# Kernel tuning notes

Hardware: AMD Instinct MI355X
Metric: run time of the kernel (lower is better)

Reference implementation:

```python
import jax, jax.numpy as jnp
import numpy as np

N, F, H, C = 8192, 256, 256, 40
LP = 0.2  # LeakyReLU slope


def setup_inputs() -> dict:
    key = jax.random.key(0)
    ks = jax.random.split(key, 11)
    s = 1.0 / np.sqrt(F)
    return {
        "x": jax.random.normal(ks[0], (N, F), jnp.float32),
        "adj_f": jax.random.uniform(ks[1], (N, N), jnp.float32) / N,
        "adj_a": jax.random.uniform(ks[2], (N, N), jnp.float32) / N,
        "Wp": jax.random.normal(ks[3], (F, F), jnp.float32) * s,
        "bp": jax.random.normal(ks[4], (F,), jnp.float32) * s,
        "Wg": jax.random.normal(ks[5], (F, F), jnp.float32) * s,
        "Wb": jax.random.normal(ks[6], (F, F), jnp.float32) * s,
        "W1": jax.random.normal(ks[7], (F, H), jnp.float32) * s,
        "b1": jax.random.normal(ks[8], (H,), jnp.float32) * s,
        "W2": jax.random.normal(ks[9], (H, C), jnp.float32) * s,
        "b2": jax.random.normal(ks[10], (C,), jnp.float32) * s,
    }


def reference(x, adj_f, adj_a, Wp, bp, Wg, Wb, W1, b1, W2, b2):
    # --- DynamicPrompt.forward ---
    # GraphConvolution: adj_f @ (x @ Wp) + bp, then ReLU
    base_prompt = jax.nn.relu(adj_f @ (x @ Wp) + bp)  # [N, F]
    # adj_a.fill_diagonal_(0)
    idx = jnp.arange(N)
    adj_a0 = adj_a.at[idx, idx].set(0.0)
    neighbor = adj_a0 @ x                             # [N, F]
    gamma = jax.nn.leaky_relu(neighbor @ Wg, LP) + 1.0
    beta = jax.nn.leaky_relu(neighbor @ Wb, LP)
    learned_prompt = gamma * base_prompt + beta
    # F.normalize: L2 along dim=1, eps=1e-12
    nrm = jnp.linalg.norm(learned_prompt, axis=1, keepdims=True)
    learned_prompt = learned_prompt / jnp.maximum(nrm, 1e-12)
    # --- mix prompt into input, run frozen teacher GCN (eval: no dropout) ---
    x_in = 0.5 * (x + learned_prompt)
    h = jax.nn.relu(adj_a @ (x_in @ W1) + b1)         # gc1
    logits = adj_a @ (h @ W2) + b2                    # gc2
    return jax.nn.log_softmax(logits, axis=1)         # [N, C]
```

## Files before the change

### kernel.cpp

```cpp
#include <hip/hip_runtime.h>

typedef unsigned short u16;
typedef __attribute__((ext_vector_type(8))) short bf16x8;
typedef __attribute__((ext_vector_type(4))) float f32x4;

__device__ __forceinline__ u16 f2bf(float f) {
  union { float f; unsigned u; } v; v.f = f;
  unsigned r = v.u + 0x7FFFu + ((v.u >> 16) & 1u);
  return (u16)(r >> 16);
}
__device__ __forceinline__ float bf2f(u16 h) {
  union { unsigned u; float f; } v; v.u = ((unsigned)h) << 16; return v.f;
}
__device__ __forceinline__ unsigned pk2(float a, float b) {
  return (unsigned)f2bf(a) | ((unsigned)f2bf(b) << 16);
}
__device__ __forceinline__ unsigned cvtpk(float a, float b) {
  unsigned r;
  asm("v_cvt_pk_bf16_f32 %0, %1, %2" : "=v"(r) : "v"(a), "v"(b));
  return r;
}
__device__ __forceinline__ void gld16(const void* g, void* l) {
  __builtin_amdgcn_global_load_lds(
      (const __attribute__((address_space(1))) unsigned int*)g,
      (__attribute__((address_space(3))) unsigned int*)l, 16, 0, 0);
}

__global__ __launch_bounds__(256)
void prep_w_k(const float* __restrict__ Wp, const float* __restrict__ Wg,
              const float* __restrict__ Wb, const float* __restrict__ W1,
              const float* __restrict__ W2, u16* __restrict__ WpT,
              u16* __restrict__ WgbT, u16* __restrict__ W1T,
              u16* __restrict__ W2T) {
  int z = blockIdx.z;
  const float* in; u16* out; int C = 256;
  if (z == 0) { in = Wp; out = WpT; }
  else if (z == 1) { in = Wg; out = WgbT; }
  else if (z == 2) { in = Wb; out = WgbT + 65536; }
  else if (z == 3) { in = W1; out = W1T; }
  else { in = W2; out = W2T; C = 40; if (blockIdx.x >= 2) return; }
  __shared__ float tile[32][33];
  int tj = blockIdx.x * 32, ti = blockIdx.y * 32;
  int t = threadIdx.x, c = t & 31, r0 = t >> 5;
#pragma unroll
  for (int p = 0; p < 4; ++p) {
    int r = r0 + p * 8;
    tile[r][c] = (tj + c < C) ? in[(size_t)(ti + r) * C + (tj + c)] : 0.f;
  }
  __syncthreads();
#pragma unroll
  for (int p = 0; p < 4; ++p) {
    int rr = r0 + p * 8;
    out[(size_t)(tj + rr) * 256 + (ti + c)] = f2bf(tile[c][rr]);
  }
}

__global__ __launch_bounds__(256)
void prep_x_k(const float* __restrict__ x, u16* __restrict__ xT,
              u16* __restrict__ xbf) {
  __shared__ float tile[32][33];
  int tj = blockIdx.x * 32, ti = blockIdx.y * 32;
  int t = threadIdx.x, c = t & 31, r0 = t >> 5;
#pragma unroll
  for (int p = 0; p < 4; ++p) {
    int r = r0 + p * 8;
    float v = x[(size_t)(ti + r) * 256 + (tj + c)];
    tile[r][c] = v;
    xbf[(size_t)(ti + r) * 256 + (tj + c)] = f2bf(v);
  }
  __syncthreads();
#pragma unroll
  for (int p = 0; p < 4; ++p) {
    int rr = r0 + p * 8;
    xT[(size_t)(tj + rr) * 8192 + (ti + c)] = f2bf(tile[c][rr]);
  }
}

__global__ __launch_bounds__(256)
void diag_k(const float* __restrict__ adj, float* __restrict__ d) {
  int i = blockIdx.x * 256 + threadIdx.x;
  d[i] = bf2f(f2bf(adj[(size_t)i * 8193]));
}

template <int BN, bool ABF, bool WRB, bool PACK>
__global__ __launch_bounds__(256, 3)
void bgemm_k(const void* __restrict__ Av, const u16* __restrict__ Bt,
             void* __restrict__ part, u16* __restrict__ Aout) {
  constexpr int BM = 64;
  constexpr int KP = 2048;
  constexpr int NSTEP = KP / 64;
  constexpr int AROWB = ABF ? 128 : 256;
  constexpr int ABYTES = BM * AROWB;
  constexpr int NA = ABYTES / 4096;
  constexpr int NB = BN * 128 / 4096;
  constexpr int FR = 2;
  constexpr int FC = BN / 32;

  __shared__ char sA[ABYTES];
  __shared__ u16 sB[BN * 64];
  const int t = threadIdx.x, lane = t & 63, w = t >> 6;
  const int l15 = lane & 15, lhi = lane >> 4;
  const int xcd = blockIdx.x & 7, idx = blockIdx.x >> 3;
  const int kp = xcd >> 1;
  const int m = (idx << 1) | (xcd & 1);
  const int mBase = m * BM;
  const int kpBase = kp * KP;
  const int waveM = (w >> 1) * 32;
  const int waveN = (w & 1) * (BN / 2);

  f32x4 acc[FR][FC];
#pragma unroll
  for (int a = 0; a < FR; ++a)
#pragma unroll
    for (int b = 0; b < FC; ++b) acc[a][b] = (f32x4){0.f, 0.f, 0.f, 0.f};

  for (int st = 0; st < NSTEP; ++st) {
    const int k0 = kpBase + st * 64;
#pragma unroll
    for (int i = 0; i < NA; ++i) {
      int L = i * 4096 + t * 16;
      int row, kb;
      if (ABF) { row = L >> 7; kb = (L & 127) ^ ((row & 7) << 4); }
      else     { row = L >> 8; kb = (L & 255) ^ ((row & 7) << 4); }
      const char* g;
      if (ABF)
        g = (const char*)Av + (((size_t)(mBase + row)) << 14) + ((size_t)k0 << 1) + kb;
      else
        g = (const char*)Av + (((size_t)(mBase + row)) << 15) + ((size_t)k0 << 2) + kb;
      gld16(g, (char*)sA + L);
    }
#pragma unroll
    for (int i = 0; i < NB; ++i) {
      int L = i * 4096 + t * 16;
      int n = L >> 7;
      int kb = (L & 127) ^ ((n & 7) << 4);
      gld16((const char*)Bt + ((size_t)n << 14) + ((size_t)k0 << 1) + kb,
            (char*)sB + L);
    }
    __syncthreads();
    if (WRB && !ABF) {
      int r = t >> 2, cb = (t & 3) << 6;
      int sw = (r & 7) << 4;
      const char* sar = (const char*)sA + r * 256;
      f32x4 v0 = *(const f32x4*)(sar + ((cb) ^ sw));
      f32x4 v1 = *(const f32x4*)(sar + ((cb + 16) ^ sw));
      f32x4 v2 = *(const f32x4*)(sar + ((cb + 32) ^ sw));
      f32x4 v3 = *(const f32x4*)(sar + ((cb + 48) ^ sw));
      uint4 q0, q1;
      q0.x = cvtpk(v0.x, v0.y); q0.y = cvtpk(v0.z, v0.w);
      q0.z = cvtpk(v1.x, v1.y); q0.w = cvtpk(v1.z, v1.w);
      q1.x = cvtpk(v2.x, v2.y); q1.y = cvtpk(v2.z, v2.w);
      q1.z = cvtpk(v3.x, v3.y); q1.w = cvtpk(v3.z, v3.w);
      u16* dst = Aout + ((size_t)(mBase + r) << 13) + k0 + (cb >> 2);
      *(uint4*)dst = q0;
      *(uint4*)(dst + 8) = q1;
    }
#pragma unroll
    for (int ks = 0; ks < 2; ++ks) {
      bf16x8 av[FR], bv[FC];
#pragma unroll
      for (int fr = 0; fr < FR; ++fr) {
        int row = waveM + fr * 16 + l15;
        if (ABF) {
          int off = row * 128 + ((ks * 64 + lhi * 16) ^ ((row & 7) << 4));
          av[fr] = *(const bf16x8*)((const char*)sA + off);
        } else {
          int inrow = ks * 128 + lhi * 32;
          int sw = (row & 7) << 4;
          const char* sar = (const char*)sA + row * 256;
          f32x4 x0 = *(const f32x4*)(sar + (inrow ^ sw));
          f32x4 x1 = *(const f32x4*)(sar + ((inrow + 16) ^ sw));
          union { bf16x8 v; unsigned u[4]; } p;
          p.u[0] = cvtpk(x0.x, x0.y); p.u[1] = cvtpk(x0.z, x0.w);
          p.u[2] = cvtpk(x1.x, x1.y); p.u[3] = cvtpk(x1.z, x1.w);
          av[fr] = p.v;
        }
      }
#pragma unroll
      for (int fc = 0; fc < FC; ++fc) {
        int n = waveN + fc * 16 + l15;
        int off = n * 128 + ((ks * 64 + lhi * 16) ^ ((n & 7) << 4));
        bv[fc] = *(const bf16x8*)((const char*)sB + off);
      }
#pragma unroll
      for (int fr = 0; fr < FR; ++fr)
#pragma unroll
        for (int fc = 0; fc < FC; ++fc)
          acc[fr][fc] = __builtin_amdgcn_mfma_f32_16x16x32_bf16(
              av[fr], bv[fc], acc[fr][fc], 0, 0, 0);
    }
    __syncthreads();
  }

  if (PACK) {
    unsigned* pp = (unsigned*)part + (size_t)kp * 8192 * 128 + (size_t)mBase * 128;
#pragma unroll
    for (int fr = 0; fr < FR; ++fr)
#pragma unroll
      for (int fcp = 0; fcp < FC / 2; ++fcp) {
        int g = (waveN >> 5) + fcp;
        int r0 = waveM + fr * 16 + lhi * 4;
#pragma unroll
        for (int j = 0; j < 4; ++j)
          pp[(size_t)(r0 + j) * 128 + g * 16 + l15] =
              cvtpk(acc[fr][2 * fcp][j], acc[fr][2 * fcp + 1][j]);
      }
  } else {
    float* pp = (float*)part + (size_t)kp * 8192 * BN + (size_t)mBase * BN;
#pragma unroll
    for (int fr = 0; fr < FR; ++fr)
#pragma unroll
      for (int fc = 0; fc < FC; ++fc) {
        int col = waveN + fc * 16 + l15;
        int r0 = waveM + fr * 16 + lhi * 4;
#pragma unroll
        for (int j = 0; j < 4; ++j)
          pp[(size_t)(r0 + j) * BN + col] = acc[fr][fc][j];
      }
  }
}

template <int BN, int EPI, int OMODE>
__global__ __launch_bounds__(256)
void sgemm_k(const u16* __restrict__ Abf, const u16* __restrict__ Bt,
             float* __restrict__ C, int ldc, u16* __restrict__ Ct) {
  __shared__ u16 sA[32 * 256];
  __shared__ u16 sB[BN * 256];
  const int t = threadIdx.x, lane = t & 63, w = t >> 6;
  const int rowBase = blockIdx.x * 32;
  const u16* bt = Bt + (size_t)blockIdx.y * BN * 256;
  const int colBlk = blockIdx.y * BN;

#pragma unroll
  for (int i = 0; i < 4; ++i) {
    int lin = ((w * 4 + i) << 10) + (lane << 4);
    int row = lin >> 9;
    int kb = (lin & 511) ^ ((row & 7) << 4);
    const char* g = (const char*)Abf + ((size_t)(rowBase + row) << 9) + kb;
    gld16(g, (char*)sA + ((w * 4 + i) << 10));
  }
#pragma unroll
  for (int i = 0; i < BN / 8; ++i) {
    int lin = ((w * (BN / 8) + i) << 10) + (lane << 4);
    int n = lin >> 9;
    int kb = (lin & 511) ^ ((n & 7) << 4);
    const char* g = (const char*)bt + ((size_t)n << 9) + kb;
    gld16(g, (char*)sB + ((w * (BN / 8) + i) << 10));
  }
  __syncthreads();

  constexpr int FC = BN / 32;
  const int waveM = (w & 1) * 16;
  const int waveN = (w >> 1) * (BN / 2);
  f32x4 acc[FC];
#pragma unroll
  for (int b = 0; b < FC; ++b) acc[b] = (f32x4){0.f, 0.f, 0.f, 0.f};

#pragma unroll
  for (int ks = 0; ks < 8; ++ks) {
    int row = waveM + (lane & 15);
    int offA = (row * 512 + ks * 64 + ((lane >> 4) * 16)) ^ ((row & 7) << 4);
    bf16x8 av = *(const bf16x8*)((const char*)sA + offA);
#pragma unroll
    for (int fc = 0; fc < FC; ++fc) {
      int n = waveN + fc * 16 + (lane & 15);
      int offB = (n * 512 + ks * 64 + ((lane >> 4) * 16)) ^ ((n & 7) << 4);
      bf16x8 bv = *(const bf16x8*)((const char*)sB + offB);
      acc[fc] = __builtin_amdgcn_mfma_f32_16x16x32_bf16(av, bv, acc[fc], 0, 0, 0);
    }
  }

#pragma unroll
  for (int fc = 0; fc < FC; ++fc) {
    int col = waveN + fc * 16 + (lane & 15);
    int r0 = rowBase + waveM + ((lane >> 4) << 2);
    float o[4];
#pragma unroll
    for (int j = 0; j < 4; ++j) {
      float xv = acc[fc][j];
      if (EPI == 1) xv = fmaxf(xv, 0.f);
      if (EPI == 2) xv = (xv > 0.f) ? xv : 0.2f * xv;
      o[j] = xv;
    }
    if (OMODE == 1) {
      uint2 q; q.x = pk2(o[0], o[1]); q.y = pk2(o[2], o[3]);
      *(uint2*)(Ct + (size_t)(colBlk + col) * 8192 + r0) = q;
    } else if (OMODE == 2) {
#pragma unroll
      for (int j = 0; j < 4; ++j)
        Ct[(size_t)(r0 + j) * ldc + colBlk + col] = f2bf(o[j]);
    } else {
#pragma unroll
      for (int j = 0; j < 4; ++j)
        C[(size_t)(r0 + j) * ldc + colBlk + col] = o[j];
    }
  }
}

template <int MODE>
__global__ __launch_bounds__(256)
void reduce4p_k(const unsigned* __restrict__ part, const float* __restrict__ bias,
                const float* __restrict__ dd, const u16* __restrict__ xbf,
                u16* __restrict__ Cb) {
  const int tid = threadIdx.x;
  const int row = blockIdx.x * 2 + (tid >> 7);
  const int uc = tid & 127;
  const size_t S = (size_t)8192 * 128;
  const size_t b = (size_t)row * 128 + uc;
  float slo = 0.f, shi = 0.f;
#pragma unroll
  for (int p = 0; p < 4; ++p) {
    unsigned v = part[b + (size_t)p * S];
    slo += bf2f((u16)(v & 0xffff));
    shi += bf2f((u16)(v >> 16));
  }
  const int clo = (uc & 15) + ((uc >> 4) << 5), chi = clo + 16;
  if (MODE == 1) {
    float d = dd[row];
    slo -= d * bf2f(xbf[(size_t)row * 256 + clo]);
    shi -= d * bf2f(xbf[(size_t)row * 256 + chi]);
  } else {
    slo = fmaxf(slo + bias[clo], 0.f);
    shi = fmaxf(shi + bias[chi], 0.f);
  }
  Cb[(size_t)row * 256 + clo] = f2bf(slo);
  Cb[(size_t)row * 256 + chi] = f2bf(shi);
}

__global__ __launch_bounds__(128)
void fuse_red_k(const unsigned* __restrict__ part, const float* __restrict__ bp,
                const u16* __restrict__ gbuf, const u16* __restrict__ xbf,
                u16* __restrict__ xin_bf) {
  const int row = blockIdx.x, uc = threadIdx.x;
  const size_t S = (size_t)8192 * 128;
  const size_t b = (size_t)row * 128 + uc;
  float slo = 0.f, shi = 0.f;
#pragma unroll
  for (int p = 0; p < 4; ++p) {
    unsigned v = part[b + (size_t)p * S];
    slo += bf2f((u16)(v & 0xffff));
    shi += bf2f((u16)(v >> 16));
  }
  const int clo = (uc & 15) + ((uc >> 4) << 5), chi = clo + 16;
  float baselo = fmaxf(slo + bp[clo], 0.f);
  float basehi = fmaxf(shi + bp[chi], 0.f);
  float glo = bf2f(gbuf[(size_t)row * 512 + clo]);
  float ghi = bf2f(gbuf[(size_t)row * 512 + chi]);
  float btlo = bf2f(gbuf[(size_t)row * 512 + 256 + clo]);
  float bthi = bf2f(gbuf[(size_t)row * 512 + 256 + chi]);
  float lplo = (glo + 1.f) * baselo + btlo;
  float lphi = (ghi + 1.f) * basehi + bthi;
  float ss = lplo * lplo + lphi * lphi;
#pragma unroll
  for (int off = 32; off >= 1; off >>= 1) ss += __shfl_xor(ss, off);
  __shared__ float wsum[2];
  if ((uc & 63) == 0) wsum[uc >> 6] = ss;
  __syncthreads();
  float inv = 1.f / fmaxf(sqrtf(wsum[0] + wsum[1]), 1e-12f);
  xin_bf[(size_t)row * 256 + clo] =
      f2bf(0.5f * (bf2f(xbf[(size_t)row * 256 + clo]) + lplo * inv));
  xin_bf[(size_t)row * 256 + chi] =
      f2bf(0.5f * (bf2f(xbf[(size_t)row * 256 + chi]) + lphi * inv));
}

__global__ __launch_bounds__(256)
void reduce_lsm_k(const float* __restrict__ part, const float* __restrict__ b2,
                  float* __restrict__ out) {
  const int t = threadIdx.x, lane = t & 63, w = t >> 6;
  const int row = blockIdx.x * 4 + w;
  const size_t i = (size_t)row * 64 + lane;
  const size_t S = (size_t)8192 * 64;
  float v = 0.f;
#pragma unroll
  for (int p = 0; p < 4; ++p) v += part[i + (size_t)p * S];
  v = (lane < 40) ? v + b2[lane] : -1e30f;
  float mx = v;
#pragma unroll
  for (int off = 32; off >= 1; off >>= 1) mx = fmaxf(mx, __shfl_xor(mx, off));
  float e = (lane < 40) ? expf(v - mx) : 0.f;
#pragma unroll
  for (int off = 32; off >= 1; off >>= 1) e += __shfl_xor(e, off);
  float ls = mx + logf(e);
  if (lane < 40) out[(size_t)row * 40 + lane] = v - ls;
}

extern "C" void kernel_launch(void* const* d_in, const int* in_sizes, int n_in,
                              void* d_out, int out_size, void* d_ws, size_t ws_size,
                              hipStream_t stream) {
  const float* x = (const float*)d_in[0];
  const float* adj_f = (const float*)d_in[1];
  const float* adj_a = (const float*)d_in[2];
  const float* Wp = (const float*)d_in[3];
  const float* bp = (const float*)d_in[4];
  const float* Wg = (const float*)d_in[5];
  const float* Wb = (const float*)d_in[6];
  const float* W1 = (const float*)d_in[7];
  const float* b1 = (const float*)d_in[8];
  const float* W2 = (const float*)d_in[9];
  const float* b2 = (const float*)d_in[10];
  float* out = (float*)d_out;

  char* ws = (char*)d_ws;
  size_t off = 0;
  auto alloc = [&](size_t bytes) {
    char* p = ws + off;
    off += (bytes + 255) & ~(size_t)255;
    return p;
  };
  unsigned* partA = (unsigned*)alloc((size_t)4 * 8192 * 128 * 4);
  unsigned* partB = (unsigned*)alloc((size_t)4 * 8192 * 128 * 4);
  float* partBF = (float*)partB;
  u16* featT = (u16*)alloc((size_t)256 * 8192 * 2);
  u16* featT64 = (u16*)alloc((size_t)64 * 8192 * 2);
  u16* xT = (u16*)alloc((size_t)256 * 8192 * 2);
  u16* xbf = (u16*)alloc((size_t)8192 * 256 * 2);
  u16* xin_bf = (u16*)alloc((size_t)8192 * 256 * 2);
  u16* neigh_bf = (u16*)alloc((size_t)8192 * 256 * 2);
  u16* h_bf = (u16*)alloc((size_t)8192 * 256 * 2);
  u16* gbuf = (u16*)alloc((size_t)8192 * 512 * 2);
  u16* WpT = (u16*)alloc(256 * 256 * 2);
  u16* WgbT = (u16*)alloc(512 * 256 * 2);
  u16* W1T = (u16*)alloc(256 * 256 * 2);
  u16* W2T = (u16*)alloc(64 * 256 * 2);
  float* dd = (float*)alloc(8192 * 4);

  const size_t adjBytes = (size_t)8192 * 8192 * 2;
  bool useBf = (ws_size >= off + adjBytes + 256);
  u16* adj_bf = useBf ? (u16*)alloc(adjBytes) : nullptr;

  dim3 b256(256);
  prep_w_k<<<dim3(8, 8, 5), b256, 0, stream>>>(Wp, Wg, Wb, W1, W2, WpT, WgbT, W1T, W2T);
  prep_x_k<<<dim3(8, 256), b256, 0, stream>>>(x, xT, xbf);
  diag_k<<<32, b256, 0, stream>>>(adj_a, dd);

  sgemm_k<128, 0, 1><<<dim3(256, 2), b256, 0, stream>>>(xbf, WpT, nullptr, 0, featT);
  bgemm_k<256, false, false, true><<<512, b256, 0, stream>>>(adj_f, featT, partA, nullptr);
  if (useBf)
    bgemm_k<256, false, true, true><<<512, b256, 0, stream>>>(adj_a, xT, partB, adj_bf);
  else
    bgemm_k<256, false, false, true><<<512, b256, 0, stream>>>(adj_a, xT, partB, nullptr);
  reduce4p_k<1><<<4096, b256, 0, stream>>>(partB, nullptr, dd, xbf, neigh_bf);
  sgemm_k<128, 2, 2><<<dim3(256, 4), b256, 0, stream>>>(neigh_bf, WgbT, nullptr, 512, gbuf);
  fuse_red_k<<<8192, dim3(128), 0, stream>>>(partA, bp, gbuf, xbf, xin_bf);
  sgemm_k<128, 0, 1><<<dim3(256, 2), b256, 0, stream>>>(xin_bf, W1T, nullptr, 0, featT);
  if (useBf)
    bgemm_k<256, true, false, true><<<512, b256, 0, stream>>>(adj_bf, featT, partB, nullptr);
  else
    bgemm_k<256, false, false, true><<<512, b256, 0, stream>>>(adj_a, featT, partB, nullptr);
  reduce4p_k<2><<<4096, b256, 0, stream>>>(partB, b1, nullptr, nullptr, h_bf);
  sgemm_k<64, 0, 1><<<dim3(256, 1), b256, 0, stream>>>(h_bf, W2T, nullptr, 0, featT64);
  if (useBf)
    bgemm_k<64, true, false, false><<<512, b256, 0, stream>>>(adj_bf, featT64, partB, nullptr);
  else
    bgemm_k<64, false, false, false><<<512, b256, 0, stream>>>(adj_a, featT64, partB, nullptr);
  reduce_lsm_k<<<2048, b256, 0, stream>>>(partBF, b2, out);
}
```

Measured before the change: 333.9 us.

## Widen bgemm to 512 threads and convert fp32 A to bf16 before LDS

```diff
diff --git a/kernel.cpp b/kernel.cpp
--- a/kernel.cpp
+++ b/kernel.cpp
@@ -83,20 +83,18 @@
 }
 
 template <int BN, bool ABF, bool WRB, bool PACK>
-__global__ __launch_bounds__(256, 3)
+__global__ __launch_bounds__(512, 4)
 void bgemm_k(const void* __restrict__ Av, const u16* __restrict__ Bt,
              void* __restrict__ part, u16* __restrict__ Aout) {
   constexpr int BM = 64;
   constexpr int KP = 2048;
   constexpr int NSTEP = KP / 64;
-  constexpr int AROWB = ABF ? 128 : 256;
-  constexpr int ABYTES = BM * AROWB;
-  constexpr int NA = ABYTES / 4096;
-  constexpr int NB = BN * 128 / 4096;
+  constexpr int MT = 8192 / BM;
+  constexpr int NB = BN * 128 / 8192;
   constexpr int FR = 2;
-  constexpr int FC = BN / 32;
-
-  __shared__ char sA[ABYTES];
+  constexpr int FC = BN / 64;
+
+  __shared__ u16 sA[BM * 64];
   __shared__ u16 sB[BN * 64];
   const int t = threadIdx.x, lane = t & 63, w = t >> 6;
   const int l15 = lane & 15, lhi = lane >> 4;
@@ -105,76 +103,53 @@
   const int m = (idx << 1) | (xcd & 1);
   const int mBase = m * BM;
   const int kpBase = kp * KP;
-  const int waveM = (w >> 1) * 32;
-  const int waveN = (w & 1) * (BN / 2);
+  const int waveM = (w >> 2) * 32;
+  const int waveN = (w & 3) * (BN / 4);
 
   f32x4 acc[FR][FC];
 #pragma unroll
   for (int a = 0; a < FR; ++a)
 #pragma unroll
     for (int b = 0; b < FC; ++b) acc[a][b] = (f32x4){0.f, 0.f, 0.f, 0.f};
+
+  const int rA = t >> 3, qA = t & 7;
 
   for (int st = 0; st < NSTEP; ++st) {
     const int k0 = kpBase + st * 64;
 #pragma unroll
-    for (int i = 0; i < NA; ++i) {
-      int L = i * 4096 + t * 16;
-      int row, kb;
-      if (ABF) { row = L >> 7; kb = (L & 127) ^ ((row & 7) << 4); }
-      else     { row = L >> 8; kb = (L & 255) ^ ((row & 7) << 4); }
-      const char* g;
-      if (ABF)
-        g = (const char*)Av + (((size_t)(mBase + row)) << 14) + ((size_t)k0 << 1) + kb;
-      else
-        g = (const char*)Av + (((size_t)(mBase + row)) << 15) + ((size_t)k0 << 2) + kb;
-      gld16(g, (char*)sA + L);
-    }
-#pragma unroll
     for (int i = 0; i < NB; ++i) {
-      int L = i * 4096 + t * 16;
+      int L = i * 8192 + t * 16;
       int n = L >> 7;
       int kb = (L & 127) ^ ((n & 7) << 4);
       gld16((const char*)Bt + ((size_t)n << 14) + ((size_t)k0 << 1) + kb,
             (char*)sB + L);
     }
+    if (ABF) {
+      int L = t * 16;
+      int row = L >> 7;
+      int kb = (L & 127) ^ ((row & 7) << 4);
+      gld16((const char*)Av + ((size_t)(mBase + row) << 14) + ((size_t)k0 << 1) + kb,
+            (char*)sA + L);
+    } else {
+      const float* gp = (const float*)Av + ((size_t)(mBase + rA) << 13) + k0 + qA * 8;
+      float4 f0 = *(const float4*)gp;
+      float4 f1 = *(const float4*)(gp + 4);
+      uint4 qq;
+      qq.x = cvtpk(f0.x, f0.y); qq.y = cvtpk(f0.z, f0.w);
+      qq.z = cvtpk(f1.x, f1.y); qq.w = cvtpk(f1.z, f1.w);
+      *(uint4*)((char*)sA + rA * 128 + ((qA * 16) ^ ((rA & 7) << 4))) = qq;
+      if (WRB)
+        *(uint4*)(Aout + ((size_t)(mBase + rA) << 13) + k0 + qA * 8) = qq;
+    }
     __syncthreads();
-    if (WRB && !ABF) {
-      int r = t >> 2, cb = (t & 3) << 6;
-      int sw = (r & 7) << 4;
-      const char* sar = (const char*)sA + r * 256;
-      f32x4 v0 = *(const f32x4*)(sar + ((cb) ^ sw));
-      f32x4 v1 = *(const f32x4*)(sar + ((cb + 16) ^ sw));
-      f32x4 v2 = *(const f32x4*)(sar + ((cb + 32) ^ sw));
-      f32x4 v3 = *(const f32x4*)(sar + ((cb + 48) ^ sw));
-      uint4 q0, q1;
-      q0.x = cvtpk(v0.x, v0.y); q0.y = cvtpk(v0.z, v0.w);
-      q0.z = cvtpk(v1.x, v1.y); q0.w = cvtpk(v1.z, v1.w);
-      q1.x = cvtpk(v2.x, v2.y); q1.y = cvtpk(v2.z, v2.w);
-      q1.z = cvtpk(v3.x, v3.y); q1.w = cvtpk(v3.z, v3.w);
-      u16* dst = Aout + ((size_t)(mBase + r) << 13) + k0 + (cb >> 2);
-      *(uint4*)dst = q0;
-      *(uint4*)(dst + 8) = q1;
-    }
 #pragma unroll
     for (int ks = 0; ks < 2; ++ks) {
       bf16x8 av[FR], bv[FC];
 #pragma unroll
       for (int fr = 0; fr < FR; ++fr) {
         int row = waveM + fr * 16 + l15;
-        if (ABF) {
-          int off = row * 128 + ((ks * 64 + lhi * 16) ^ ((row & 7) << 4));
-          av[fr] = *(const bf16x8*)((const char*)sA + off);
-        } else {
-          int inrow = ks * 128 + lhi * 32;
-          int sw = (row & 7) << 4;
-          const char* sar = (const char*)sA + row * 256;
-          f32x4 x0 = *(const f32x4*)(sar + (inrow ^ sw));
-          f32x4 x1 = *(const f32x4*)(sar + ((inrow + 16) ^ sw));
-          union { bf16x8 v; unsigned u[4]; } p;
-          p.u[0] = cvtpk(x0.x, x0.y); p.u[1] = cvtpk(x0.z, x0.w);
-          p.u[2] = cvtpk(x1.x, x1.y); p.u[3] = cvtpk(x1.z, x1.w);
-          av[fr] = p.v;
-        }
+        int off = row * 128 + ((ks * 64 + lhi * 16) ^ ((row & 7) << 4));
+        av[fr] = *(const bf16x8*)((const char*)sA + off);
       }
 #pragma unroll
       for (int fc = 0; fc < FC; ++fc) {
@@ -428,30 +403,30 @@
   bool useBf = (ws_size >= off + adjBytes + 256);
   u16* adj_bf = useBf ? (u16*)alloc(adjBytes) : nullptr;
 
-  dim3 b256(256);
+  dim3 b256(256), b512(512);
   prep_w_k<<<dim3(8, 8, 5), b256, 0, stream>>>(Wp, Wg, Wb, W1, W2, WpT, WgbT, W1T, W2T);
   prep_x_k<<<dim3(8, 256), b256, 0, stream>>>(x, xT, xbf);
   diag_k<<<32, b256, 0, stream>>>(adj_a, dd);
 
   sgemm_k<128, 0, 1><<<dim3(256, 2), b256, 0, stream>>>(xbf, WpT, nullptr, 0, featT);
-  bgemm_k<256, false, false, true><<<512, b256, 0, stream>>>(adj_f, featT, partA, nullptr);
+  bgemm_k<256, false, false, true><<<512, b512, 0, stream>>>(adj_f, featT, partA, nullptr);
   if (useBf)
-    bgemm_k<256, false, true, true><<<512, b256, 0, stream>>>(adj_a, xT, partB, adj_bf);
+    bgemm_k<256, false, true, true><<<512, b512, 0, stream>>>(adj_a, xT, partB, adj_bf);
   else
-    bgemm_k<256, false, false, true><<<512, b256, 0, stream>>>(adj_a, xT, partB, nullptr);
+    bgemm_k<256, false, false, true><<<512, b512, 0, stream>>>(adj_a, xT, partB, nullptr);
   reduce4p_k<1><<<4096, b256, 0, stream>>>(partB, nullptr, dd, xbf, neigh_bf);
   sgemm_k<128, 2, 2><<<dim3(256, 4), b256, 0, stream>>>(neigh_bf, WgbT, nullptr, 512, gbuf);
   fuse_red_k<<<8192, dim3(128), 0, stream>>>(partA, bp, gbuf, xbf, xin_bf);
   sgemm_k<128, 0, 1><<<dim3(256, 2), b256, 0, stream>>>(xin_bf, W1T, nullptr, 0, featT);
   if (useBf)
-    bgemm_k<256, true, false, true><<<512, b256, 0, stream>>>(adj_bf, featT, partB, nullptr);
+    bgemm_k<256, true, false, true><<<512, b512, 0, stream>>>(adj_bf, featT, partB, nullptr);
   else
-    bgemm_k<256, false, false, true><<<512, b256, 0, stream>>>(adj_a, featT, partB, nullptr);
+    bgemm_k<256, false, false, true><<<512, b512, 0, stream>>>(adj_a, featT, partB, nullptr);
   reduce4p_k<2><<<4096, b256, 0, stream>>>(partB, b1, nullptr, nullptr, h_bf);
   sgemm_k<64, 0, 1><<<dim3(256, 1), b256, 0, stream>>>(h_bf, W2T, nullptr, 0, featT64);
   if (useBf)
-    bgemm_k<64, true, false, false><<<512, b256, 0, stream>>>(adj_bf, featT64, partB, nullptr);
+    bgemm_k<64, true, false, false><<<512, b512, 0, stream>>>(adj_bf, featT64, partB, nullptr);
   else
-    bgemm_k<64, false, false, false><<<512, b256, 0, stream>>>(adj_a, featT64, partB, nullptr);
+    bgemm_k<64, false, false, false><<<512, b512, 0, stream>>>(adj_a, featT64, partB, nullptr);
   reduce_lsm_k<<<2048, b256, 0, stream>>>(partBF, b2, out);
 }
```

Result: no change. 334.1 us (+0.1%).
